# Optimization experiments

Hardware: AMD Instinct MI355X
Metric: run time of the kernel (lower is better)

The kernel has to match this reference:

```python
import jax, jax.numpy as jnp
import numpy as np

HEADS = 8
DIM_HEAD = 64
SCALE = DIM_HEAD ** -0.5


def setup_inputs() -> dict:
    key = jax.random.key(0)
    k1, k2, k3, k4 = jax.random.split(key, 4)
    b, dim, l = 4, 256, 2048
    hidden = HEADS * DIM_HEAD  # 512
    x = jax.random.normal(k1, (b, dim, l), dtype=jnp.float32)
    w_qkv = jax.random.normal(k2, (3 * hidden, dim), dtype=jnp.float32) * (dim ** -0.5)
    w_out = jax.random.normal(k3, (dim, hidden), dtype=jnp.float32) * (hidden ** -0.5)
    b_out = jax.random.normal(k4, (dim,), dtype=jnp.float32) * 0.01
    return {"x": x, "w_qkv": w_qkv, "w_out": w_out, "b_out": b_out}


def reference(x, w_qkv, w_out, b_out):
    b, c, l = x.shape
    hidden = HEADS * DIM_HEAD
    # 1x1 conv == pointwise linear over channels
    qkv = jnp.einsum('oc,bcl->bol', w_qkv, x)  # [b, 3*hidden, l]
    q, k, v = jnp.split(qkv, 3, axis=1)
    def to_heads(t):
        return t.reshape(b, HEADS, DIM_HEAD, l)  # b h d l
    q, k, v = to_heads(q), to_heads(k), to_heads(v)
    q = q * SCALE
    sim = jnp.einsum('bhdi,bhdj->bhij', q, k)      # [b, h, l, l]
    attn = jax.nn.softmax(sim, axis=-1)
    out = jnp.einsum('bhij,bhdj->bhid', attn, v)   # [b, h, l, d]
    out = out.transpose(0, 1, 3, 2).reshape(b, hidden, l)  # b (h d) l
    return jnp.einsum('oc,bcl->bol', w_out, out) + b_out[None, :, None]
```

## Files before the change

### kernel.cpp

```cpp
#include <hip/hip_runtime.h>
#include <math.h>

#define Bn   4
#define Cc   256
#define Ll   2048
#define Hh   8
#define Dd   64
#define HID  512
#define OQKV 1536

#define QSCALE 0.18033688011112042f
#define ESHIFT 4.328085122666891f

typedef _Float16 half4v __attribute__((ext_vector_type(4)));
typedef _Float16 half8v __attribute__((ext_vector_type(8)));
typedef __fp16   fp16x2 __attribute__((ext_vector_type(2)));
typedef float    f32x16 __attribute__((ext_vector_type(16)));
typedef unsigned uint2v __attribute__((ext_vector_type(2)));

__device__ __forceinline__ void gload_lds16(const _Float16* g, _Float16* l) {
  __builtin_amdgcn_global_load_lds(
      (const __attribute__((address_space(1))) void*)g,
      (__attribute__((address_space(3))) void*)l, 16, 0, 0);
}

__device__ inline unsigned pkrtz(float a, float b) {
  union { fp16x2 h; unsigned u; } v;
  v.h = __builtin_amdgcn_cvt_pkrtz(a, b);
  return v.u;
}

__global__ __launch_bounds__(256) void conv_xTw(const float* __restrict__ x,
                                                const float* __restrict__ wqkv,
                                                const float* __restrict__ wout,
                                                _Float16* __restrict__ xT,
                                                _Float16* __restrict__ wqkvh,
                                                _Float16* __restrict__ wouth) {
  __shared__ _Float16 T[64][72];
  const int l0 = blockIdx.x * 64, c0 = blockIdx.y * 64, bz = blockIdx.z;
  const int t = threadIdx.x;
  {
    int gid = (((blockIdx.z * gridDim.y + blockIdx.y) * gridDim.x + blockIdx.x) << 8) + t;
    int nthr = (gridDim.x * gridDim.y * gridDim.z) << 8;
    for (int i = gid; i < OQKV * Cc; i += nthr) {
      float v = wqkv[i];
      if (i < HID * Cc) v *= QSCALE;
      wqkvh[i] = (_Float16)v;
    }
    for (int i = gid; i < Cc * HID; i += nthr) wouth[i] = (_Float16)wout[i];
  }
  const float* xb = x + ((size_t)bz * Cc + c0) * Ll + l0;
  {
    int cl = t >> 2, lq = (t & 3) * 16;
#pragma unroll
    for (int i = 0; i < 16; i += 4) {
      float4 v = *(const float4*)&xb[(size_t)cl * Ll + lq + i];
      T[lq + i + 0][cl] = (_Float16)v.x;
      T[lq + i + 1][cl] = (_Float16)v.y;
      T[lq + i + 2][cl] = (_Float16)v.z;
      T[lq + i + 3][cl] = (_Float16)v.w;
    }
  }
  __syncthreads();
  {
    int ll = t >> 2, cq = (t & 3) * 16;
    _Float16* dst = xT + ((size_t)bz * Ll + l0 + ll) * Cc + c0 + cq;
    *(half8v*)&dst[0] = *(const half8v*)&T[ll][cq];
    *(half8v*)&dst[8] = *(const half8v*)&T[ll][cq + 8];
  }
}

__global__ __launch_bounds__(256) void gemmT(const _Float16* __restrict__ xT,
                                             const _Float16* __restrict__ Wqk,
                                             _Float16* __restrict__ qkT) {
  __shared__ _Float16 As[64][64];
  __shared__ _Float16 Bs[64][64];
  const int bz = blockIdx.z;
  const int m0 = blockIdx.y * 64;
  const int n0 = blockIdx.x * 64;
  const int t = threadIdx.x;
  const int w = t >> 6, lane = t & 63, lid = lane & 31, lh = lane >> 5;
  const int mw = (w >> 1) * 32, nw = (w & 1) * 32;
  const _Float16* Ab = xT + (size_t)bz * Ll * Cc;
  const int srow = lane >> 3;
  const int sgr  = ((lane & 7) ^ srow) << 3;

  f32x16 acc;
#pragma unroll
  for (int r = 0; r < 16; ++r) acc[r] = 0.0f;

  for (int k0 = 0; k0 < Cc; k0 += 64) {
#pragma unroll
    for (int q = 0; q < 2; ++q) {
      const int r0 = (q * 4 + w) * 8;
      gload_lds16(&Ab[(size_t)(m0 + r0 + srow) * Cc + k0 + sgr], &As[r0][0]);
      gload_lds16(&Wqk[(size_t)(n0 + r0 + srow) * Cc + k0 + sgr], &Bs[r0][0]);
    }
    __syncthreads();
    const int rk = lid & 7;
#pragma unroll
    for (int kq = 0; kq < 4; ++kq) {
      const int co = ((2 * kq + lh) ^ rk) << 3;
      half8v af = *(const half8v*)&As[mw + lid][co];
      half8v bf = *(const half8v*)&Bs[nw + lid][co];
      acc = __builtin_amdgcn_mfma_f32_32x32x16_f16(af, bf, acc, 0, 0, 0);
    }
    __syncthreads();
  }
#pragma unroll
  for (int r = 0; r < 16; ++r) {
    const int row = m0 + mw + (r & 3) + 8 * (r >> 2) + 4 * lh;
    const int col = n0 + nw + lid;
    qkT[((size_t)bz * Ll + row) * 1024 + col] = (_Float16)acc[r];
  }
}

template <int MODE>
__global__ __launch_bounds__(256) void gemm64(
    const _Float16* __restrict__ A, const _Float16* __restrict__ B,
    const float* __restrict__ bias, void* __restrict__ C, int M, int K) {
  __shared__ _Float16 As[64][64];
  __shared__ _Float16 Bs[64][64];
  const int bz = blockIdx.z;
  const int m0 = blockIdx.y * 64, n0 = blockIdx.x * 64;
  const int t = threadIdx.x;
  const int w = t >> 6, lane = t & 63, lid = lane & 31, lh = lane >> 5;
  const int mw = (w >> 1) * 32, nw = (w & 1) * 32;
  const _Float16* Bb = B + (size_t)bz * (size_t)Ll * K;
  const int srow = lane >> 3;
  const int sgr  = ((lane & 7) ^ srow) << 3;

  f32x16 acc;
#pragma unroll
  for (int r = 0; r < 16; ++r) acc[r] = 0.0f;

  for (int k0 = 0; k0 < K; k0 += 64) {
#pragma unroll
    for (int q = 0; q < 2; ++q) {
      const int r0 = (q * 4 + w) * 8;
      gload_lds16(&A[(size_t)(m0 + r0 + srow) * K + k0 + sgr], &As[r0][0]);
      gload_lds16(&Bb[(size_t)(n0 + r0 + srow) * K + k0 + sgr], &Bs[r0][0]);
    }
    __syncthreads();
    const int rk = lid & 7;
#pragma unroll
    for (int kq = 0; kq < 4; ++kq) {
      const int co = ((2 * kq + lh) ^ rk) << 3;
      half8v af = *(const half8v*)&As[mw + lid][co];
      half8v bf = *(const half8v*)&Bs[nw + lid][co];
      acc = __builtin_amdgcn_mfma_f32_32x32x16_f16(af, bf, acc, 0, 0, 0);
    }
    __syncthreads();
  }
#pragma unroll
  for (int r = 0; r < 16; ++r) {
    const int row = m0 + mw + (r & 3) + 8 * (r >> 2) + 4 * lh;
    const int col = n0 + nw + lid;
    if (MODE == 1) {
      ((float*)C)[((size_t)bz * M + row) * Ll + col] = acc[r] + bias[row];
    } else {
      ((_Float16*)C)[((size_t)bz * M + row) * Ll + col] = (_Float16)acc[r];
    }
  }
}

__global__ __launch_bounds__(512, 4) void attn_f16(const _Float16* __restrict__ qkT,
                                                   const _Float16* __restrict__ vh,
                                                   _Float16* __restrict__ aoutT) {
  __shared__ __align__(16) char lds_raw[34816];
  _Float16 (*Ks)[64][64] = (_Float16 (*)[64][64])(lds_raw);
  _Float16 (*Vs)[64][64] = (_Float16 (*)[64][64])(lds_raw + 16384);

  const int n = blockIdx.x;
  const int xcd = n & 7;
  const int xt = (n >> 3) & 15;
  const int gs = n >> 7;
  const int g = gs * 8 + xcd;
  const int h = g & 7, b = g >> 3;
  const int i0 = xt * 128;

  const int t = threadIdx.x;
  const int w = t >> 6, lane = t & 63, lid = lane & 31, lh = lane >> 5;
  const int wg = w & 3;
  const int wj = w >> 2;
  const _Float16* qrow  = qkT + (size_t)b * Ll * 1024;
  const _Float16* kbase = qrow + 512;
  const _Float16* vbase = vh + ((size_t)b * HID + h * Dd) * Ll;

  half8v qf[4];
  {
    const _Float16* q0 = &qrow[(size_t)(i0 + 32 * wg + lid) * 1024 + h * Dd + 8 * lh];
#pragma unroll
    for (int kq = 0; kq < 4; ++kq)
      qf[kq] = *(const half8v*)&q0[kq * 16];
  }

  const bool isK = w < 4;
  const int sw = isK ? w : w - 4;
  const int srow = lane >> 3;
  const int sgr  = ((lane & 7) ^ srow) << 3;

#pragma unroll
  for (int q = 0; q < 2; ++q) {
    const int r0 = (q * 4 + sw) * 8;
    if (isK)
      gload_lds16(&kbase[(size_t)(r0 + srow) * 1024 + h * Dd + sgr], &Ks[0][r0][0]);
    else
      gload_lds16(&vbase[(size_t)(r0 + srow) * Ll + sgr], &Vs[0][r0][0]);
  }
  __syncthreads();

  float lsum = 0.0f;
  f32x16 oacc[2];
#pragma unroll
  for (int ds = 0; ds < 2; ++ds)
#pragma unroll
    for (int r = 0; r < 16; ++r) oacc[ds][r] = 0.0f;

  const int rk = lid & 7;
  const int krow = wj * 32 + lid;

  for (int j0 = 0; j0 < Ll; j0 += 64) {
    const int cur = (j0 >> 6) & 1;
    const int nj = j0 + 64;
    const bool more = nj < Ll;

    if (more) {
      const int nb = cur ^ 1;
#pragma unroll
      for (int q = 0; q < 2; ++q) {
        const int r0 = (q * 4 + sw) * 8;
        if (isK)
          gload_lds16(&kbase[(size_t)(nj + r0 + srow) * 1024 + h * Dd + sgr], &Ks[nb][r0][0]);
        else
          gload_lds16(&vbase[(size_t)(r0 + srow) * Ll + nj + sgr], &Vs[nb][r0][0]);
      }
    }

    f32x16 s;
#pragma unroll
    for (int r = 0; r < 16; ++r) s[r] = -ESHIFT;
    __builtin_amdgcn_s_setprio(1);
#pragma unroll
    for (int kq = 0; kq < 4; ++kq) {
      half8v kf = *(const half8v*)&Ks[cur][krow][((2 * kq + lh) ^ rk) << 3];
      s = __builtin_amdgcn_mfma_f32_32x32x16_f16(kf, qf[kq], s, 0, 0, 0);
    }
    __builtin_amdgcn_s_setprio(0);
    unsigned W[8];
#pragma unroll
    for (int q = 0; q < 4; ++q) {
      float p0 = __builtin_amdgcn_exp2f(s[4 * q + 0]);
      float p1 = __builtin_amdgcn_exp2f(s[4 * q + 1]);
      float p2 = __builtin_amdgcn_exp2f(s[4 * q + 2]);
      float p3 = __builtin_amdgcn_exp2f(s[4 * q + 3]);
      lsum += (p0 + p1) + (p2 + p3);
      W[2 * q]     = pkrtz(p0, p1);
      W[2 * q + 1] = pkrtz(p2, p3);
    }
#pragma unroll
    for (int f = 0; f < 2; ++f) {
      uint2v r02 = __builtin_amdgcn_permlane32_swap(W[4 * f + 0], W[4 * f + 2], false, false);
      uint2v r13 = __builtin_amdgcn_permlane32_swap(W[4 * f + 1], W[4 * f + 3], false, false);
      union { unsigned u[4]; half8v hv; } pu;
      pu.u[0] = r02[0];
      pu.u[1] = r13[0];
      pu.u[2] = r02[1];
      pu.u[3] = r13[1];
      const int jq = 2 * wj + f;
      __builtin_amdgcn_s_setprio(1);
#pragma unroll
      for (int ds = 0; ds < 2; ++ds) {
        half8v vf = *(const half8v*)&Vs[cur][ds * 32 + lid][((2 * jq + lh) ^ rk) << 3];
        oacc[ds] = __builtin_amdgcn_mfma_f32_32x32x16_f16(vf, pu.hv, oacc[ds], 0, 0, 0);
      }
      __builtin_amdgcn_s_setprio(0);
    }

    if (more) __syncthreads();
  }

  lsum += __shfl_xor(lsum, 32);
  __syncthreads();
  float* red = (float*)lds_raw;
  const int rbase = ((wg << 6) + lane) * 33;
  if (wj == 1) {
#pragma unroll
    for (int ds = 0; ds < 2; ++ds)
#pragma unroll
      for (int r = 0; r < 16; ++r) red[rbase + ds * 16 + r] = oacc[ds][r];
    red[rbase + 32] = lsum;
  }
  __syncthreads();
  if (wj == 0) {
#pragma unroll
    for (int ds = 0; ds < 2; ++ds)
#pragma unroll
      for (int r = 0; r < 16; ++r) oacc[ds][r] += red[rbase + ds * 16 + r];
    lsum += red[rbase + 32];
    float inv = 1.0f / lsum;
    _Float16* dst = aoutT + ((size_t)b * Ll + i0 + 32 * wg + lid) * HID + h * Dd;
#pragma unroll
    for (int ds = 0; ds < 2; ++ds)
#pragma unroll
      for (int g2 = 0; g2 < 4; ++g2) {
        int d = ds * 32 + 8 * g2 + 4 * lh;
        half4v o;
#pragma unroll
        for (int c = 0; c < 4; ++c) o[c] = (_Float16)(oacc[ds][4 * g2 + c] * inv);
        *(half4v*)&dst[d] = o;
      }
  }
}

extern "C" void kernel_launch(void* const* d_in, const int* in_sizes, int n_in,
                              void* d_out, int out_size, void* d_ws, size_t ws_size,
                              hipStream_t stream) {
  const float* x     = (const float*)d_in[0];
  const float* w_qkv = (const float*)d_in[1];
  const float* w_out = (const float*)d_in[2];
  const float* b_out = (const float*)d_in[3];
  float* out = (float*)d_out;

  char* ws = (char*)d_ws;
  _Float16* xT     = (_Float16*)(ws);
  _Float16* wqkvh  = (_Float16*)(ws + 4194304);
  _Float16* wouth  = (_Float16*)(ws + 4980736);
  _Float16* qkT    = (_Float16*)(ws + 5242880);
  _Float16* vh     = (_Float16*)(ws + 22020096);
  _Float16* aoutT  = (_Float16*)(ws + 30408704);

  dim3 blk(256);
  conv_xTw<<<dim3(Ll / 64, Cc / 64, Bn), blk, 0, stream>>>(x, w_qkv, w_out, xT, wqkvh, wouth);
  gemmT<<<dim3(1024 / 64, Ll / 64, Bn), blk, 0, stream>>>(xT, wqkvh, qkT);
  gemm64<0><<<dim3(Ll / 64, HID / 64, Bn), blk, 0, stream>>>(
      wqkvh + (size_t)2 * HID * Cc, xT, nullptr, vh, HID, Cc);
  attn_f16<<<dim3(512, 1, 1), dim3(512), 0, stream>>>(qkT, vh, aoutT);
  gemm64<1><<<dim3(Ll / 64, Cc / 64, Bn), blk, 0, stream>>>(
      wouth, aoutT, b_out, out, Cc, HID);
}
```

Baseline: 140.1 us.

## Merge QK and V projection GEMMs and widen attention KV tiles to 128

The separate QK and V projection GEMM launches become one kernel that dispatches on block index, which removes a launch and lets both run in one grid. The attention kernel now stages 128 keys/values per iteration, as two 64-row halves in a double-buffered 64KB dynamic LDS region, so it needs half as many barrier-separated iterations. The cost is more LDS per block, which can limit how many blocks fit on a CU, and a one-time host-side attribute call to allow the larger dynamic shared memory.

```diff
diff --git a/kernel.cpp b/kernel.cpp
--- a/kernel.cpp
+++ b/kernel.cpp
@@ -70,18 +70,29 @@
   }
 }
 
-__global__ __launch_bounds__(256) void gemmT(const _Float16* __restrict__ xT,
-                                             const _Float16* __restrict__ Wqk,
-                                             _Float16* __restrict__ qkT) {
+__global__ __launch_bounds__(256) void qkv_fused(const _Float16* __restrict__ xT,
+                                                 const _Float16* __restrict__ wqkvh,
+                                                 _Float16* __restrict__ qkT,
+                                                 _Float16* __restrict__ vh) {
   __shared__ _Float16 As[64][64];
   __shared__ _Float16 Bs[64][64];
-  const int bz = blockIdx.z;
-  const int m0 = blockIdx.y * 64;
-  const int n0 = blockIdx.x * 64;
+  const int id = blockIdx.x, bz = blockIdx.z;
+  const _Float16 *Ap, *Bp;
+  _Float16* outp;
+  int m0, n0, rs;
+  if (id < 512) {
+    Ap = xT + (size_t)bz * Ll * Cc;     m0 = (id >> 4) * 64;
+    Bp = wqkvh;                         n0 = (id & 15) * 64;
+    outp = qkT + (size_t)bz * Ll * 1024; rs = 1024;
+  } else {
+    const int id2 = id - 512;
+    Ap = wqkvh + (size_t)2 * HID * Cc;  m0 = (id2 >> 5) * 64;
+    Bp = xT + (size_t)bz * Ll * Cc;     n0 = (id2 & 31) * 64;
+    outp = vh + (size_t)bz * HID * Ll;  rs = Ll;
+  }
   const int t = threadIdx.x;
   const int w = t >> 6, lane = t & 63, lid = lane & 31, lh = lane >> 5;
   const int mw = (w >> 1) * 32, nw = (w & 1) * 32;
-  const _Float16* Ab = xT + (size_t)bz * Ll * Cc;
   const int srow = lane >> 3;
   const int sgr  = ((lane & 7) ^ srow) << 3;
 
@@ -93,8 +104,8 @@
 #pragma unroll
     for (int q = 0; q < 2; ++q) {
       const int r0 = (q * 4 + w) * 8;
-      gload_lds16(&Ab[(size_t)(m0 + r0 + srow) * Cc + k0 + sgr], &As[r0][0]);
-      gload_lds16(&Wqk[(size_t)(n0 + r0 + srow) * Cc + k0 + sgr], &Bs[r0][0]);
+      gload_lds16(&Ap[(size_t)(m0 + r0 + srow) * Cc + k0 + sgr], &As[r0][0]);
+      gload_lds16(&Bp[(size_t)(n0 + r0 + srow) * Cc + k0 + sgr], &Bs[r0][0]);
     }
     __syncthreads();
     const int rk = lid & 7;
@@ -111,14 +122,14 @@
   for (int r = 0; r < 16; ++r) {
     const int row = m0 + mw + (r & 3) + 8 * (r >> 2) + 4 * lh;
     const int col = n0 + nw + lid;
-    qkT[((size_t)bz * Ll + row) * 1024 + col] = (_Float16)acc[r];
-  }
-}
-
-template <int MODE>
-__global__ __launch_bounds__(256) void gemm64(
-    const _Float16* __restrict__ A, const _Float16* __restrict__ B,
-    const float* __restrict__ bias, void* __restrict__ C, int M, int K) {
+    outp[(size_t)row * rs + col] = (_Float16)acc[r];
+  }
+}
+
+__global__ __launch_bounds__(256) void gemm_out(const _Float16* __restrict__ A,
+                                                const _Float16* __restrict__ B,
+                                                const float* __restrict__ bias,
+                                                float* __restrict__ C) {
   __shared__ _Float16 As[64][64];
   __shared__ _Float16 Bs[64][64];
   const int bz = blockIdx.z;
@@ -126,7 +137,7 @@
   const int t = threadIdx.x;
   const int w = t >> 6, lane = t & 63, lid = lane & 31, lh = lane >> 5;
   const int mw = (w >> 1) * 32, nw = (w & 1) * 32;
-  const _Float16* Bb = B + (size_t)bz * (size_t)Ll * K;
+  const _Float16* Bb = B + (size_t)bz * (size_t)Ll * HID;
   const int srow = lane >> 3;
   const int sgr  = ((lane & 7) ^ srow) << 3;
 
@@ -134,12 +145,12 @@
 #pragma unroll
   for (int r = 0; r < 16; ++r) acc[r] = 0.0f;
 
-  for (int k0 = 0; k0 < K; k0 += 64) {
+  for (int k0 = 0; k0 < HID; k0 += 64) {
 #pragma unroll
     for (int q = 0; q < 2; ++q) {
       const int r0 = (q * 4 + w) * 8;
-      gload_lds16(&A[(size_t)(m0 + r0 + srow) * K + k0 + sgr], &As[r0][0]);
-      gload_lds16(&Bb[(size_t)(n0 + r0 + srow) * K + k0 + sgr], &Bs[r0][0]);
+      gload_lds16(&A[(size_t)(m0 + r0 + srow) * HID + k0 + sgr], &As[r0][0]);
+      gload_lds16(&Bb[(size_t)(n0 + r0 + srow) * HID + k0 + sgr], &Bs[r0][0]);
     }
     __syncthreads();
     const int rk = lid & 7;
@@ -156,20 +167,16 @@
   for (int r = 0; r < 16; ++r) {
     const int row = m0 + mw + (r & 3) + 8 * (r >> 2) + 4 * lh;
     const int col = n0 + nw + lid;
-    if (MODE == 1) {
-      ((float*)C)[((size_t)bz * M + row) * Ll + col] = acc[r] + bias[row];
-    } else {
-      ((_Float16*)C)[((size_t)bz * M + row) * Ll + col] = (_Float16)acc[r];
-    }
+    C[((size_t)bz * Cc + row) * Ll + col] = acc[r] + bias[row];
   }
 }
 
 __global__ __launch_bounds__(512, 4) void attn_f16(const _Float16* __restrict__ qkT,
                                                    const _Float16* __restrict__ vh,
                                                    _Float16* __restrict__ aoutT) {
-  __shared__ __align__(16) char lds_raw[34816];
-  _Float16 (*Ks)[64][64] = (_Float16 (*)[64][64])(lds_raw);
-  _Float16 (*Vs)[64][64] = (_Float16 (*)[64][64])(lds_raw + 16384);
+  extern __shared__ __align__(16) char lds_raw[];
+  _Float16 (*Ks)[2][64][64] = (_Float16 (*)[2][64][64])(lds_raw);
+  _Float16 (*Vs)[2][64][64] = (_Float16 (*)[2][64][64])(lds_raw + 32768);
 
   const int n = blockIdx.x;
   const int xcd = n & 7;
@@ -201,13 +208,17 @@
   const int sgr  = ((lane & 7) ^ srow) << 3;
 
 #pragma unroll
-  for (int q = 0; q < 2; ++q) {
-    const int r0 = (q * 4 + sw) * 8;
-    if (isK)
-      gload_lds16(&kbase[(size_t)(r0 + srow) * 1024 + h * Dd + sgr], &Ks[0][r0][0]);
-    else
-      gload_lds16(&vbase[(size_t)(r0 + srow) * Ll + sgr], &Vs[0][r0][0]);
-  }
+  for (int jh = 0; jh < 2; ++jh)
+#pragma unroll
+    for (int q = 0; q < 2; ++q) {
+      const int r0 = (q * 4 + sw) * 8;
+      if (isK)
+        gload_lds16(&kbase[(size_t)(jh * 64 + r0 + srow) * 1024 + h * Dd + sgr],
+                    &Ks[0][jh][r0][0]);
+      else
+        gload_lds16(&vbase[(size_t)(r0 + srow) * Ll + jh * 64 + sgr],
+                    &Vs[0][jh][r0][0]);
+    }
   __syncthreads();
 
   float lsum = 0.0f;
@@ -220,61 +231,68 @@
   const int rk = lid & 7;
   const int krow = wj * 32 + lid;
 
-  for (int j0 = 0; j0 < Ll; j0 += 64) {
-    const int cur = (j0 >> 6) & 1;
-    const int nj = j0 + 64;
+  for (int j0 = 0; j0 < Ll; j0 += 128) {
+    const int cur = (j0 >> 7) & 1;
+    const int nj = j0 + 128;
     const bool more = nj < Ll;
 
     if (more) {
       const int nb = cur ^ 1;
 #pragma unroll
-      for (int q = 0; q < 2; ++q) {
-        const int r0 = (q * 4 + sw) * 8;
-        if (isK)
-          gload_lds16(&kbase[(size_t)(nj + r0 + srow) * 1024 + h * Dd + sgr], &Ks[nb][r0][0]);
-        else
-          gload_lds16(&vbase[(size_t)(r0 + srow) * Ll + nj + sgr], &Vs[nb][r0][0]);
-      }
-    }
-
-    f32x16 s;
-#pragma unroll
-    for (int r = 0; r < 16; ++r) s[r] = -ESHIFT;
-    __builtin_amdgcn_s_setprio(1);
-#pragma unroll
-    for (int kq = 0; kq < 4; ++kq) {
-      half8v kf = *(const half8v*)&Ks[cur][krow][((2 * kq + lh) ^ rk) << 3];
-      s = __builtin_amdgcn_mfma_f32_32x32x16_f16(kf, qf[kq], s, 0, 0, 0);
-    }
-    __builtin_amdgcn_s_setprio(0);
-    unsigned W[8];
-#pragma unroll
-    for (int q = 0; q < 4; ++q) {
-      float p0 = __builtin_amdgcn_exp2f(s[4 * q + 0]);
-      float p1 = __builtin_amdgcn_exp2f(s[4 * q + 1]);
-      float p2 = __builtin_amdgcn_exp2f(s[4 * q + 2]);
-      float p3 = __builtin_amdgcn_exp2f(s[4 * q + 3]);
-      lsum += (p0 + p1) + (p2 + p3);
-      W[2 * q]     = pkrtz(p0, p1);
-      W[2 * q + 1] = pkrtz(p2, p3);
-    }
-#pragma unroll
-    for (int f = 0; f < 2; ++f) {
-      uint2v r02 = __builtin_amdgcn_permlane32_swap(W[4 * f + 0], W[4 * f + 2], false, false);
-      uint2v r13 = __builtin_amdgcn_permlane32_swap(W[4 * f + 1], W[4 * f + 3], false, false);
-      union { unsigned u[4]; half8v hv; } pu;
-      pu.u[0] = r02[0];
-      pu.u[1] = r13[0];
-      pu.u[2] = r02[1];
-      pu.u[3] = r13[1];
-      const int jq = 2 * wj + f;
+      for (int jh = 0; jh < 2; ++jh)
+#pragma unroll
+        for (int q = 0; q < 2; ++q) {
+          const int r0 = (q * 4 + sw) * 8;
+          if (isK)
+            gload_lds16(&kbase[(size_t)(nj + jh * 64 + r0 + srow) * 1024 + h * Dd + sgr],
+                        &Ks[nb][jh][r0][0]);
+          else
+            gload_lds16(&vbase[(size_t)(r0 + srow) * Ll + nj + jh * 64 + sgr],
+                        &Vs[nb][jh][r0][0]);
+        }
+    }
+
+#pragma unroll
+    for (int jh = 0; jh < 2; ++jh) {
+      f32x16 s;
+#pragma unroll
+      for (int r = 0; r < 16; ++r) s[r] = -ESHIFT;
       __builtin_amdgcn_s_setprio(1);
 #pragma unroll
-      for (int ds = 0; ds < 2; ++ds) {
-        half8v vf = *(const half8v*)&Vs[cur][ds * 32 + lid][((2 * jq + lh) ^ rk) << 3];
-        oacc[ds] = __builtin_amdgcn_mfma_f32_32x32x16_f16(vf, pu.hv, oacc[ds], 0, 0, 0);
+      for (int kq = 0; kq < 4; ++kq) {
+        half8v kf = *(const half8v*)&Ks[cur][jh][krow][((2 * kq + lh) ^ rk) << 3];
+        s = __builtin_amdgcn_mfma_f32_32x32x16_f16(kf, qf[kq], s, 0, 0, 0);
       }
       __builtin_amdgcn_s_setprio(0);
+      unsigned W[8];
+#pragma unroll
+      for (int q = 0; q < 4; ++q) {
+        float p0 = __builtin_amdgcn_exp2f(s[4 * q + 0]);
+        float p1 = __builtin_amdgcn_exp2f(s[4 * q + 1]);
+        float p2 = __builtin_amdgcn_exp2f(s[4 * q + 2]);
+        float p3 = __builtin_amdgcn_exp2f(s[4 * q + 3]);
+        lsum += (p0 + p1) + (p2 + p3);
+        W[2 * q]     = pkrtz(p0, p1);
+        W[2 * q + 1] = pkrtz(p2, p3);
+      }
+#pragma unroll
+      for (int f = 0; f < 2; ++f) {
+        uint2v r02 = __builtin_amdgcn_permlane32_swap(W[4 * f + 0], W[4 * f + 2], false, false);
+        uint2v r13 = __builtin_amdgcn_permlane32_swap(W[4 * f + 1], W[4 * f + 3], false, false);
+        union { unsigned u[4]; half8v hv; } pu;
+        pu.u[0] = r02[0];
+        pu.u[1] = r13[0];
+        pu.u[2] = r02[1];
+        pu.u[3] = r13[1];
+        const int jq = 2 * wj + f;
+        __builtin_amdgcn_s_setprio(1);
+#pragma unroll
+        for (int ds = 0; ds < 2; ++ds) {
+          half8v vf = *(const half8v*)&Vs[cur][jh][ds * 32 + lid][((2 * jq + lh) ^ rk) << 3];
+          oacc[ds] = __builtin_amdgcn_mfma_f32_32x32x16_f16(vf, pu.hv, oacc[ds], 0, 0, 0);
+        }
+        __builtin_amdgcn_s_setprio(0);
+      }
     }
 
     if (more) __syncthreads();
@@ -330,12 +348,16 @@
   _Float16* vh     = (_Float16*)(ws + 22020096);
   _Float16* aoutT  = (_Float16*)(ws + 30408704);
 
+  static bool lds_cfg = false;
+  if (!lds_cfg) {
+    hipFuncSetAttribute((const void*)attn_f16,
+                        hipFuncAttributeMaxDynamicSharedMemorySize, 65536);
+    lds_cfg = true;
+  }
+
   dim3 blk(256);
   conv_xTw<<<dim3(Ll / 64, Cc / 64, Bn), blk, 0, stream>>>(x, w_qkv, w_out, xT, wqkvh, wouth);
-  gemmT<<<dim3(1024 / 64, Ll / 64, Bn), blk, 0, stream>>>(xT, wqkvh, qkT);
-  gemm64<0><<<dim3(Ll / 64, HID / 64, Bn), blk, 0, stream>>>(
-      wqkvh + (size_t)2 * HID * Cc, xT, nullptr, vh, HID, Cc);
-  attn_f16<<<dim3(512, 1, 1), dim3(512), 0, stream>>>(qkT, vh, aoutT);
-  gemm64<1><<<dim3(Ll / 64, Cc / 64, Bn), blk, 0, stream>>>(
-      wouth, aoutT, b_out, out, Cc, HID);
-}
+  qkv_fused<<<dim3(768, 1, Bn), blk, 0, stream>>>(xT, wqkvh, qkT, vh);
+  attn_f16<<<dim3(512, 1, 1), dim3(512), 65536, stream>>>(qkT, vh, aoutT);
+  gemm_out<<<dim3(Ll / 64, Cc / 64, Bn), blk, 0, stream>>>(wouth, aoutT, b_out, out);
+}
```

Result: no change. 141.7 us (+1.2%).
